# Kernel tuning notes

Measured on AMD Instinct MI355X. Metric: run time of the kernel, lower is better.

The kernel has to match this reference:

```python
import jax, jax.numpy as jnp
import numpy as np

N = 50000      # nodes
E = 800000     # edges
D_IN = 128     # input feature dim
HID = 64       # out_channels (per-head dim; concat=False -> head mean)
HEADS = 2
NEG_SLOPE = 0.2


def gat_layer(x, src, dst, Ws, Wd, a_s, a_d, b):
    # PyG GATConv, add_self_loops=False, concat=False (mean over heads)
    n = x.shape[0]
    H, C = a_s.shape
    hs = (x @ Ws).reshape(n, H, C)          # source-side features [N,H,C]
    hd = (x @ Wd).reshape(n, H, C)          # dest-side features   [N,H,C]
    als = (hs * a_s).sum(-1)                # [N,H]
    ald = (hd * a_d).sum(-1)                # [N,H]
    e = jax.nn.leaky_relu(als[src] + ald[dst], NEG_SLOPE)   # [E,H]
    # segment softmax over edges grouped by destination node
    m = jax.ops.segment_max(e, dst, num_segments=n)
    m = jax.lax.stop_gradient(jnp.where(jnp.isfinite(m), m, 0.0))
    ex = jnp.exp(e - m[dst])
    den = jax.ops.segment_sum(ex, dst, num_segments=n)
    alpha = ex / (den[dst] + 1e-16)                          # [E,H]
    out = jax.ops.segment_sum(hs[src] * alpha[:, :, None], dst, num_segments=n)
    return out.mean(axis=1) + b             # [N,C]


def setup_inputs() -> dict:
    key = jax.random.key(0)
    ks = jax.random.split(key, 32)
    d = {}
    d["x"] = jax.random.normal(ks[0], (N, D_IN), jnp.float32)
    d["edge_index"] = jax.random.randint(ks[1], (2, E), 0, N, jnp.int32)
    dins = [D_IN, HID, HID]
    i = 2
    for l in range(1, 4):
        din = dins[l - 1]
        s = 1.0 / np.sqrt(din)
        d[f"Ws{l}"] = jax.random.normal(ks[i], (din, HEADS * HID), jnp.float32) * s; i += 1
        d[f"Wd{l}"] = jax.random.normal(ks[i], (din, HEADS * HID), jnp.float32) * s; i += 1
        d[f"as{l}"] = jax.random.normal(ks[i], (HEADS, HID), jnp.float32) * 0.1; i += 1
        d[f"ad{l}"] = jax.random.normal(ks[i], (HEADS, HID), jnp.float32) * 0.1; i += 1
        d[f"b{l}"] = jnp.zeros((HID,), jnp.float32)
        d[f"Wl{l}"] = jax.random.normal(ks[i], (din, HID), jnp.float32) * s; i += 1
        d[f"bl{l}"] = jnp.zeros((HID,), jnp.float32)
    return d


def reference(x, edge_index,
              Ws1, Wd1, as1, ad1, b1, Wl1, bl1,
              Ws2, Wd2, as2, ad2, b2, Wl2, bl2,
              Ws3, Wd3, as3, ad3, b3, Wl3, bl3):
    src, dst = edge_index[0], edge_index[1]
    h = jax.nn.relu(gat_layer(x, src, dst, Ws1, Wd1, as1, ad1, b1) + x @ Wl1 + bl1)
    h = jax.nn.relu(gat_layer(h, src, dst, Ws2, Wd2, as2, ad2, b2) + h @ Wl2 + bl2)
    h = jax.nn.relu(gat_layer(h, src, dst, Ws3, Wd3, as3, ad3, b3) + h @ Wl3 + bl3)
    return h
```

## Files before the change

kernel.cpp:

```cpp
#include <hip/hip_runtime.h>
#include <hip/hip_bf16.h>

#define NN 50000
#define NE 800000
#define SCAN_BS 1024
#define SCAN_NB ((NN + SCAN_BS - 1) / SCAN_BS)
#define EB ((NE + 255) / 256)

typedef __attribute__((ext_vector_type(8))) __bf16 bf16x8;
typedef __attribute__((ext_vector_type(4))) float float4v;

__device__ __forceinline__ unsigned pack_bf2(float lo, float hi) {
    union { __bf16 b; unsigned short u; } a, c;
    a.b = (__bf16)lo; c.b = (__bf16)hi;
    return (unsigned)a.u | ((unsigned)c.u << 16);
}
__device__ __forceinline__ float2 unpack_bf2(unsigned v) {
    union { unsigned short u; __bf16 b; } lo, hi;
    lo.u = (unsigned short)(v & 0xffff); hi.u = (unsigned short)(v >> 16);
    return make_float2((float)lo.b, (float)hi.b);
}


__device__ __forceinline__ void convert_w_part(const float* __restrict__ Ws,
                                               const float* __restrict__ Wd,
                                               const float* __restrict__ Wl,
                                               __bf16* __restrict__ Wt, int K, int i)
{
    if (i >= 320 * K) return;
    int c = i / K, k = i % K;
    float v;
    if (c < 128)      v = Ws[k * 128 + c];
    else if (c < 256) v = Wd[k * 128 + (c - 128)];
    else              v = Wl[k * 64 + (c - 256)];
    Wt[i] = (__bf16)v;
}

__global__ void __launch_bounds__(256)
prep_kernel(const int* __restrict__ ei, int* __restrict__ deg, int* __restrict__ rank,
            const float* __restrict__ Ws1, const float* __restrict__ Wd1,
            const float* __restrict__ Wl1, __bf16* __restrict__ Wt1,
            const float* __restrict__ Ws2, const float* __restrict__ Wd2,
            const float* __restrict__ Wl2, __bf16* __restrict__ Wt2,
            const float* __restrict__ Ws3, const float* __restrict__ Wd3,
            const float* __restrict__ Wl3, __bf16* __restrict__ Wt3)
{
    int bi = blockIdx.x;
    if (bi < EB) {
        int e = bi * 256 + threadIdx.x;
        if (e < NE) rank[e] = atomicAdd(&deg[ei[NE + e]], 1);
    } else if (bi < EB + 160) {
        convert_w_part(Ws1, Wd1, Wl1, Wt1, 128, (bi - EB) * 256 + threadIdx.x);
    } else if (bi < EB + 240) {
        convert_w_part(Ws2, Wd2, Wl2, Wt2, 64, (bi - EB - 160) * 256 + threadIdx.x);
    } else {
        convert_w_part(Ws3, Wd3, Wl3, Wt3, 64, (bi - EB - 240) * 256 + threadIdx.x);
    }
}


__global__ void __launch_bounds__(SCAN_BS)
scan1_kernel(const int* __restrict__ deg, int* __restrict__ exl, int* __restrict__ bsum)
{
    __shared__ int sh[SCAN_BS];
    int t = threadIdx.x;
    int i = blockIdx.x * SCAN_BS + t;
    int v = (i < NN) ? deg[i] : 0;
    sh[t] = v;
    __syncthreads();
    for (int off = 1; off < SCAN_BS; off <<= 1) {
        int u = (t >= off) ? sh[t - off] : 0;
        __syncthreads();
        sh[t] += u;
        __syncthreads();
    }
    if (i < NN) exl[i] = sh[t] - v;
    if (t == SCAN_BS - 1) bsum[blockIdx.x] = sh[t];
}

__global__ void __launch_bounds__(64)
scan2_kernel(const int* __restrict__ bsum, int* __restrict__ boff, int* __restrict__ row)
{
    int l = threadIdx.x;
    int v = (l < SCAN_NB) ? bsum[l] : 0;
    int own = v;
    for (int off = 1; off < 64; off <<= 1) {
        int u = __shfl_up(v, off);
        if (l >= off) v += u;
    }
    if (l < SCAN_NB) boff[l] = v - own;
    if (l == 63) row[NN] = v;
}

__global__ void __launch_bounds__(SCAN_BS)
scan3_kernel(const int* __restrict__ exl, const int* __restrict__ boff,
             int* __restrict__ row)
{
    int i = blockIdx.x * SCAN_BS + threadIdx.x;
    if (i >= NN) return;
    row[i] = exl[i] + boff[blockIdx.x];
}

__global__ void __launch_bounds__(256)
scatter_kernel(const int* __restrict__ ei, const int* __restrict__ rank,
               const int* __restrict__ row, int* __restrict__ csr_src)
{
    int e = blockIdx.x * 256 + threadIdx.x;
    if (e >= NE) return;
    int s = ei[e], d = ei[NE + e];
    int p = row[d] + rank[e];
    csr_src[p] = s;
}


__device__ __forceinline__ bf16x8 load_af(const __bf16* p) { return *(const bf16x8*)p; }
__device__ __forceinline__ bf16x8 load_af(const float* p) {
    float4 u = *(const float4*)p;
    float4 v = *(const float4*)(p + 4);
    bf16x8 r;
    r[0] = (__bf16)u.x; r[1] = (__bf16)u.y; r[2] = (__bf16)u.z; r[3] = (__bf16)u.w;
    r[4] = (__bf16)v.x; r[5] = (__bf16)v.y; r[6] = (__bf16)v.z; r[7] = (__bf16)v.w;
    return r;
}

template <int K, typename TIN>
__global__ void __launch_bounds__(256)
mfma_gemm(const TIN* __restrict__ xin, const __bf16* __restrict__ Wt,
          const float* __restrict__ a_s, const float* __restrict__ a_d,
          unsigned* __restrict__ hsb, float* __restrict__ lin,
          float* __restrict__ als, float* __restrict__ ald)
{
    __shared__ __align__(16) char ldsW[320 * 144];

    const int tid  = threadIdx.x;
    const int lane = tid & 63;
    const int wave = tid >> 6;
    const int l15 = lane & 15, quad = lane >> 4;
    const int nblk0 = blockIdx.x * 64;
    const int n0 = nblk0 + wave * 16;
    const int nA = min(n0 + l15, NN - 1);

    bf16x8 afr[K / 32];
#pragma unroll
    for (int ks = 0; ks < K / 32; ++ks)
        afr[ks] = load_af(xin + (size_t)nA * K + ks * 32 + quad * 8);

    float4v acc[20];
#pragma unroll
    for (int t = 0; t < 20; ++t) acc[t] = (float4v){0.f, 0.f, 0.f, 0.f};

#pragma unroll
    for (int h = 0; h < K / 64; ++h) {
        uint4 tmp[10];
#pragma unroll
        for (int i = 0; i < 10; ++i) {
            int idx = i * 256 + tid;
            int r = idx >> 3, c = idx & 7;
            tmp[i] = *(const uint4*)(Wt + (size_t)r * K + h * 64 + c * 8);
        }
        if (h) __syncthreads();
#pragma unroll
        for (int i = 0; i < 10; ++i) {
            int idx = i * 256 + tid;
            int r = idx >> 3, c = idx & 7;
            *(uint4*)&ldsW[r * 144 + c * 16] = tmp[i];
        }
        __syncthreads();

#pragma unroll
        for (int ksh = 0; ksh < 2; ++ksh) {
            int ks = h * 2 + ksh;
#pragma unroll
            for (int t = 0; t < 20; ++t) {
                bf16x8 bf = *(const bf16x8*)&ldsW[(t * 16 + l15) * 144 + (ksh * 4 + quad) * 16];
                acc[t] = __builtin_amdgcn_mfma_f32_16x16x32_bf16(afr[ks], bf, acc[t], 0, 0, 0);
            }
        }
    }

    float s0[4], s1[4], d0[4], d1[4];
#pragma unroll
    for (int r = 0; r < 4; ++r) { s0[r] = 0.f; s1[r] = 0.f; d0[r] = 0.f; d1[r] = 0.f; }
#pragma unroll
    for (int t = 0; t < 4; ++t) {
        float as0 = a_s[t * 16 + l15];
        float as1 = a_s[64 + t * 16 + l15];
        float ad0 = a_d[t * 16 + l15];
        float ad1 = a_d[64 + t * 16 + l15];
#pragma unroll
        for (int r = 0; r < 4; ++r) {
            s0[r] += acc[t][r] * as0;
            s1[r] += acc[t + 4][r] * as1;
            d0[r] += acc[t + 8][r] * ad0;
            d1[r] += acc[t + 12][r] * ad1;
        }
    }
#pragma unroll
    for (int m = 1; m < 16; m <<= 1) {
#pragma unroll
        for (int r = 0; r < 4; ++r) {
            s0[r] += __shfl_xor(s0[r], m);
            s1[r] += __shfl_xor(s1[r], m);
            d0[r] += __shfl_xor(d0[r], m);
            d1[r] += __shfl_xor(d1[r], m);
        }
    }

    __syncthreads();
    unsigned* hs_l  = (unsigned*)ldsW;
    float*    lin_l = (float*)(ldsW + 64 * 68 * 4);
    float*    al_l  = (float*)(ldsW + 2 * 64 * 68 * 4);

#pragma unroll
    for (int t = 0; t < 4; ++t) {
#pragma unroll
        for (int r = 0; r < 4; ++r) {
            int ln = wave * 16 + quad * 4 + r;
            hs_l[ln * 68 + t * 16 + l15] = pack_bf2(acc[t][r], acc[t + 4][r]);
            lin_l[ln * 68 + t * 16 + l15] = acc[t + 16][r];
        }
    }
    if (l15 == 0) {
#pragma unroll
        for (int r = 0; r < 4; ++r) {
            int ln = wave * 16 + quad * 4 + r;
            al_l[0 * 64 + ln] = s0[r];
            al_l[1 * 64 + ln] = s1[r];
            al_l[2 * 64 + ln] = d0[r];
            al_l[3 * 64 + ln] = d1[r];
        }
    }
    __syncthreads();

#pragma unroll
    for (int it = 0; it < 4; ++it) {
        int idx4 = it * 256 + tid;
        int ln = idx4 >> 4, c4 = idx4 & 15;
        int n = nblk0 + ln;
        if (n < NN) {
            *(uint4*)&hsb[(size_t)n * 64 + c4 * 4] =
                *(const uint4*)&hs_l[ln * 68 + c4 * 4];
            *(float4*)&lin[(size_t)n * 64 + c4 * 4] =
                *(const float4*)&lin_l[ln * 68 + c4 * 4];
        }
    }
    {
        int half = tid >> 7;
        int t2 = tid & 127;
        int ln = t2 >> 1, h = t2 & 1;
        int n = nblk0 + ln;
        if (n < NN) {
            float v = al_l[(half * 2 + h) * 64 + ln];
            if (half == 0) als[n * 2 + h] = v;
            else           ald[n * 2 + h] = v;
        }
    }
}


__device__ __forceinline__ float2 edge_w(const float* __restrict__ als, int s,
                                         float ad0, float ad1)
{
    float2 al = *(const float2*)&als[s * 2];
    float e0 = al.x + ad0; e0 = (e0 >= 0.f) ? e0 : 0.2f * e0;
    float e1 = al.y + ad1; e1 = (e1 >= 0.f) ? e1 : 0.2f * e1;
    return make_float2(__expf(e0), __expf(e1));
}

__device__ __forceinline__ void store_q(float* p, float v0, float v1, float v2, float v3) {
    *(float4*)p = make_float4(v0, v1, v2, v3);
}
__device__ __forceinline__ void store_q(__bf16* p, float v0, float v1, float v2, float v3) {
    *(uint2*)p = make_uint2(pack_bf2(v0, v1), pack_bf2(v2, v3));
}

template <typename TO>
__global__ void __launch_bounds__(256)
gat_aggregate(const int* __restrict__ row, const int* __restrict__ csr_src,
              const float* __restrict__ als, const float* __restrict__ ald,
              const unsigned* __restrict__ hsb, const float* __restrict__ lin,
              const float* __restrict__ b, const float* __restrict__ bl,
              TO* __restrict__ out)
{
    int w = (blockIdx.x * 256 + threadIdx.x) >> 6;
    int lane = threadIdx.x & 63;
    int q = lane >> 4;
    int l15 = lane & 15;
    if (w >= NN) return;
    int p0 = row[w], p1 = row[w + 1];
    float ad0 = ald[w * 2 + 0];
    float ad1 = ald[w * 2 + 1];

    float a0[4] = {0.f, 0.f, 0.f, 0.f};
    float a1[4] = {0.f, 0.f, 0.f, 0.f};
    float den0 = 0.f, den1 = 0.f;

    int p = p0 + q;
    for (; p + 12 < p1; p += 16) {
        int sA = csr_src[p];
        int sB = csr_src[p + 4];
        int sC = csr_src[p + 8];
        int sD = csr_src[p + 12];
        float2 eA = edge_w(als, sA, ad0, ad1);
        float2 eB = edge_w(als, sB, ad0, ad1);
        float2 eC = edge_w(als, sC, ad0, ad1);
        float2 eD = edge_w(als, sD, ad0, ad1);
        uint4 gA = *(const uint4*)&hsb[(size_t)sA * 64 + 4 * l15];
        uint4 gB = *(const uint4*)&hsb[(size_t)sB * 64 + 4 * l15];
        uint4 gC = *(const uint4*)&hsb[(size_t)sC * 64 + 4 * l15];
        uint4 gD = *(const uint4*)&hsb[(size_t)sD * 64 + 4 * l15];
        den0 += (eA.x + eB.x) + (eC.x + eD.x);
        den1 += (eA.y + eB.y) + (eC.y + eD.y);
        float2 h;
        h = unpack_bf2(gA.x); a0[0] += eA.x * h.x; a1[0] += eA.y * h.y;
        h = unpack_bf2(gA.y); a0[1] += eA.x * h.x; a1[1] += eA.y * h.y;
        h = unpack_bf2(gA.z); a0[2] += eA.x * h.x; a1[2] += eA.y * h.y;
        h = unpack_bf2(gA.w); a0[3] += eA.x * h.x; a1[3] += eA.y * h.y;
        h = unpack_bf2(gB.x); a0[0] += eB.x * h.x; a1[0] += eB.y * h.y;
        h = unpack_bf2(gB.y); a0[1] += eB.x * h.x; a1[1] += eB.y * h.y;
        h = unpack_bf2(gB.z); a0[2] += eB.x * h.x; a1[2] += eB.y * h.y;
        h = unpack_bf2(gB.w); a0[3] += eB.x * h.x; a1[3] += eB.y * h.y;
        h = unpack_bf2(gC.x); a0[0] += eC.x * h.x; a1[0] += eC.y * h.y;
        h = unpack_bf2(gC.y); a0[1] += eC.x * h.x; a1[1] += eC.y * h.y;
        h = unpack_bf2(gC.z); a0[2] += eC.x * h.x; a1[2] += eC.y * h.y;
        h = unpack_bf2(gC.w); a0[3] += eC.x * h.x; a1[3] += eC.y * h.y;
        h = unpack_bf2(gD.x); a0[0] += eD.x * h.x; a1[0] += eD.y * h.y;
        h = unpack_bf2(gD.y); a0[1] += eD.x * h.x; a1[1] += eD.y * h.y;
        h = unpack_bf2(gD.z); a0[2] += eD.x * h.x; a1[2] += eD.y * h.y;
        h = unpack_bf2(gD.w); a0[3] += eD.x * h.x; a1[3] += eD.y * h.y;
    }
    for (; p + 4 < p1; p += 8) {
        int sA = csr_src[p];
        int sB = csr_src[p + 4];
        float2 eA = edge_w(als, sA, ad0, ad1);
        float2 eB = edge_w(als, sB, ad0, ad1);
        uint4 gA = *(const uint4*)&hsb[(size_t)sA * 64 + 4 * l15];
        uint4 gB = *(const uint4*)&hsb[(size_t)sB * 64 + 4 * l15];
        den0 += eA.x + eB.x;
        den1 += eA.y + eB.y;
        float2 h;
        h = unpack_bf2(gA.x); a0[0] += eA.x * h.x; a1[0] += eA.y * h.y;
        h = unpack_bf2(gA.y); a0[1] += eA.x * h.x; a1[1] += eA.y * h.y;
        h = unpack_bf2(gA.z); a0[2] += eA.x * h.x; a1[2] += eA.y * h.y;
        h = unpack_bf2(gA.w); a0[3] += eA.x * h.x; a1[3] += eA.y * h.y;
        h = unpack_bf2(gB.x); a0[0] += eB.x * h.x; a1[0] += eB.y * h.y;
        h = unpack_bf2(gB.y); a0[1] += eB.x * h.x; a1[1] += eB.y * h.y;
        h = unpack_bf2(gB.z); a0[2] += eB.x * h.x; a1[2] += eB.y * h.y;
        h = unpack_bf2(gB.w); a0[3] += eB.x * h.x; a1[3] += eB.y * h.y;
    }
    for (; p < p1; p += 4) {
        int s = csr_src[p];
        float2 e = edge_w(als, s, ad0, ad1);
        uint4 g = *(const uint4*)&hsb[(size_t)s * 64 + 4 * l15];
        den0 += e.x; den1 += e.y;
        float2 h;
        h = unpack_bf2(g.x); a0[0] += e.x * h.x; a1[0] += e.y * h.y;
        h = unpack_bf2(g.y); a0[1] += e.x * h.x; a1[1] += e.y * h.y;
        h = unpack_bf2(g.z); a0[2] += e.x * h.x; a1[2] += e.y * h.y;
        h = unpack_bf2(g.w); a0[3] += e.x * h.x; a1[3] += e.y * h.y;
    }

#pragma unroll
    for (int i = 0; i < 4; ++i) {
        a0[i] += __shfl_xor(a0[i], 16); a0[i] += __shfl_xor(a0[i], 32);
        a1[i] += __shfl_xor(a1[i], 16); a1[i] += __shfl_xor(a1[i], 32);
    }
    den0 += __shfl_xor(den0, 16); den0 += __shfl_xor(den0, 32);
    den1 += __shfl_xor(den1, 16); den1 += __shfl_xor(den1, 32);

    if (q == 0) {
        int c0 = 4 * l15;
        float r0 = 1.f / (den0 + 1e-16f);
        float r1 = 1.f / (den1 + 1e-16f);
        float4 lv = *(const float4*)&lin[(size_t)w * 64 + c0];
        float v0 = 0.5f * (a0[0] * r0 + a1[0] * r1) + b[c0 + 0] + bl[c0 + 0] + lv.x;
        float v1 = 0.5f * (a0[1] * r0 + a1[1] * r1) + b[c0 + 1] + bl[c0 + 1] + lv.y;
        float v2 = 0.5f * (a0[2] * r0 + a1[2] * r1) + b[c0 + 2] + bl[c0 + 2] + lv.z;
        float v3 = 0.5f * (a0[3] * r0 + a1[3] * r1) + b[c0 + 3] + bl[c0 + 3] + lv.w;
        store_q(&out[(size_t)w * 64 + c0],
                fmaxf(v0, 0.f), fmaxf(v1, 0.f), fmaxf(v2, 0.f), fmaxf(v3, 0.f));
    }
}


extern "C" void kernel_launch(void* const* d_in, const int* in_sizes, int n_in,
                              void* d_out, int out_size, void* d_ws, size_t ws_size,
                              hipStream_t stream)
{
    const float* x  = (const float*)d_in[0];
    const int*   ei = (const int*)d_in[1];
    const float* Ws[3]; const float* Wd[3]; const float* As[3]; const float* Ad[3];
    const float* Bb[3]; const float* Wl[3]; const float* Bl[3];
    for (int l = 0; l < 3; ++l) {
        int base = 2 + 7 * l;
        Ws[l] = (const float*)d_in[base + 0];
        Wd[l] = (const float*)d_in[base + 1];
        As[l] = (const float*)d_in[base + 2];
        Ad[l] = (const float*)d_in[base + 3];
        Bb[l] = (const float*)d_in[base + 4];
        Wl[l] = (const float*)d_in[base + 5];
        Bl[l] = (const float*)d_in[base + 6];
    }

    float* ws = (float*)d_ws;
    unsigned* hsb = (unsigned*)ws;
    float* lin  = (float*)(hsb + (size_t)NN * 64);
    float* als  = lin + (size_t)NN * 64;
    float* ald  = als + (size_t)NN * 2;
    __bf16* hb  = (__bf16*)(ald + (size_t)NN * 2);
    __bf16* Wt1 = hb + (size_t)NN * 64;
    __bf16* Wt2 = Wt1 + 320 * 128;
    __bf16* Wt3 = Wt2 + 320 * 64;
    int* row     = (int*)(Wt3 + 320 * 64);
    int* deg     = row + (NN + 1);
    int* rank    = deg + NN;
    int* exl     = rank + NE;
    int* bsum    = exl + NN;
    int* boff    = bsum + SCAN_NB;
    int* csr_src = boff + SCAN_NB;

    const int WB  = (NN * 64 + 255) / 256;
    const int GB  = (NN + 63) / 64;

    hipMemsetAsync(deg, 0, sizeof(int) * NN, stream);
    prep_kernel<<<EB + 320, 256, 0, stream>>>(ei, deg, rank,
        Ws[0], Wd[0], Wl[0], Wt1,
        Ws[1], Wd[1], Wl[1], Wt2,
        Ws[2], Wd[2], Wl[2], Wt3);
    scan1_kernel<<<SCAN_NB, SCAN_BS, 0, stream>>>(deg, exl, bsum);
    scan2_kernel<<<1, 64, 0, stream>>>(bsum, boff, row);
    scan3_kernel<<<SCAN_NB, SCAN_BS, 0, stream>>>(exl, boff, row);
    scatter_kernel<<<EB, 256, 0, stream>>>(ei, rank, row, csr_src);

    for (int l = 0; l < 3; ++l) {
        if (l == 0) {
            mfma_gemm<128, float><<<GB, 256, 0, stream>>>(
                x, Wt1, As[0], Ad[0], hsb, lin, als, ald);
        } else {
            const __bf16* wt = (l == 1) ? Wt2 : Wt3;
            mfma_gemm<64, __bf16><<<GB, 256, 0, stream>>>(
                hb, wt, As[l], Ad[l], hsb, lin, als, ald);
        }
        if (l == 2) {
            gat_aggregate<float><<<WB, 256, 0, stream>>>(
                row, csr_src, als, ald, hsb, lin, Bb[l], Bl[l], (float*)d_out);
        } else {
            gat_aggregate<__bf16><<<WB, 256, 0, stream>>>(
                row, csr_src, als, ald, hsb, lin, Bb[l], Bl[l], hb);
        }
    }
}
```

Baseline: 340.3 us.

## Fuse CSR scan stages and scatter into GEMM launch, load weights directly

Merges scan1 and scan2 into one kernel using a last-block ticket, and folds scan3 and the edge scatter into extra blocks of the first-layer GEMM launch. This removes three kernel launches and their serialization gaps. The GEMM also drops the LDS staging of weights and reads B fragments straight from global memory, relying on cache since every block reads the same small weight matrix. Risks: more global loads per MFMA and extra block types in the first GEMM grid.

```diff
diff --git a/kernel.cpp b/kernel.cpp
--- a/kernel.cpp
+++ b/kernel.cpp
@@ -6,6 +6,8 @@
 #define SCAN_BS 1024
 #define SCAN_NB ((NN + SCAN_BS - 1) / SCAN_BS)
 #define EB ((NE + 255) / 256)
+#define GB ((NN + 63) / 64)
+#define RB ((NN + 1 + 255) / 256)
 
 typedef __attribute__((ext_vector_type(8))) __bf16 bf16x8;
 typedef __attribute__((ext_vector_type(4))) float float4v;
@@ -60,9 +62,11 @@
 
 
 __global__ void __launch_bounds__(SCAN_BS)
-scan1_kernel(const int* __restrict__ deg, int* __restrict__ exl, int* __restrict__ bsum)
+scan12_kernel(const int* __restrict__ deg, int* __restrict__ exl,
+              int* __restrict__ bsum, int* __restrict__ boff, int* __restrict__ ticket)
 {
     __shared__ int sh[SCAN_BS];
+    __shared__ int lastFlag;
     int t = threadIdx.x;
     int i = blockIdx.x * SCAN_BS + t;
     int v = (i < NN) ? deg[i] : 0;
@@ -75,41 +79,23 @@
         __syncthreads();
     }
     if (i < NN) exl[i] = sh[t] - v;
-    if (t == SCAN_BS - 1) bsum[blockIdx.x] = sh[t];
-}
-
-__global__ void __launch_bounds__(64)
-scan2_kernel(const int* __restrict__ bsum, int* __restrict__ boff, int* __restrict__ row)
-{
-    int l = threadIdx.x;
-    int v = (l < SCAN_NB) ? bsum[l] : 0;
-    int own = v;
-    for (int off = 1; off < 64; off <<= 1) {
-        int u = __shfl_up(v, off);
-        if (l >= off) v += u;
-    }
-    if (l < SCAN_NB) boff[l] = v - own;
-    if (l == 63) row[NN] = v;
-}
-
-__global__ void __launch_bounds__(SCAN_BS)
-scan3_kernel(const int* __restrict__ exl, const int* __restrict__ boff,
-             int* __restrict__ row)
-{
-    int i = blockIdx.x * SCAN_BS + threadIdx.x;
-    if (i >= NN) return;
-    row[i] = exl[i] + boff[blockIdx.x];
-}
-
-__global__ void __launch_bounds__(256)
-scatter_kernel(const int* __restrict__ ei, const int* __restrict__ rank,
-               const int* __restrict__ row, int* __restrict__ csr_src)
-{
-    int e = blockIdx.x * 256 + threadIdx.x;
-    if (e >= NE) return;
-    int s = ei[e], d = ei[NE + e];
-    int p = row[d] + rank[e];
-    csr_src[p] = s;
+    if (t == SCAN_BS - 1) {
+        bsum[blockIdx.x] = sh[t];
+        __threadfence();
+        lastFlag = (atomicAdd(ticket, 1) == SCAN_NB - 1);
+    }
+    __syncthreads();
+    if (lastFlag && t < 64) {
+        __threadfence();
+        int l = t;
+        int bv = (l < SCAN_NB) ? bsum[l] : 0;
+        int own = bv;
+        for (int off = 1; off < 64; off <<= 1) {
+            int u = __shfl_up(bv, off);
+            if (l >= off) bv += u;
+        }
+        if (l < SCAN_NB) boff[l] = bv - own;
+    }
 }
 
 
@@ -123,16 +109,36 @@
     return r;
 }
 
-template <int K, typename TIN>
+template <int K, typename TIN, bool FUSE>
 __global__ void __launch_bounds__(256)
 mfma_gemm(const TIN* __restrict__ xin, const __bf16* __restrict__ Wt,
           const float* __restrict__ a_s, const float* __restrict__ a_d,
           unsigned* __restrict__ hsb, float* __restrict__ lin,
-          float* __restrict__ als, float* __restrict__ ald)
-{
-    __shared__ __align__(16) char ldsW[320 * 144];
-
-    const int tid  = threadIdx.x;
+          float* __restrict__ als, float* __restrict__ ald,
+          const int* __restrict__ ei, const int* __restrict__ rank,
+          const int* __restrict__ exl, const int* __restrict__ boff,
+          int* __restrict__ row, int* __restrict__ csr_src)
+{
+    const int tid = threadIdx.x;
+
+    if (FUSE && blockIdx.x >= GB) {
+        int bi = blockIdx.x - GB;
+        if (bi < RB) {
+            int i = bi * 256 + tid;
+            if (i < NN)       row[i] = exl[i] + boff[i >> 10];
+            else if (i == NN) row[i] = NE;
+        } else {
+            int e = (bi - RB) * 256 + tid;
+            if (e < NE) {
+                int s = ei[e], d = ei[NE + e];
+                csr_src[exl[d] + boff[d >> 10] + rank[e]] = s;
+            }
+        }
+        return;
+    }
+
+    __shared__ __align__(16) char ldsE[2 * 64 * 68 * 4 + 1024];
+
     const int lane = tid & 63;
     const int wave = tid >> 6;
     const int l15 = lane & 15, quad = lane >> 4;
@@ -149,32 +155,13 @@
 #pragma unroll
     for (int t = 0; t < 20; ++t) acc[t] = (float4v){0.f, 0.f, 0.f, 0.f};
 
-#pragma unroll
-    for (int h = 0; h < K / 64; ++h) {
-        uint4 tmp[10];
-#pragma unroll
-        for (int i = 0; i < 10; ++i) {
-            int idx = i * 256 + tid;
-            int r = idx >> 3, c = idx & 7;
-            tmp[i] = *(const uint4*)(Wt + (size_t)r * K + h * 64 + c * 8);
-        }
-        if (h) __syncthreads();
-#pragma unroll
-        for (int i = 0; i < 10; ++i) {
-            int idx = i * 256 + tid;
-            int r = idx >> 3, c = idx & 7;
-            *(uint4*)&ldsW[r * 144 + c * 16] = tmp[i];
-        }
-        __syncthreads();
-
-#pragma unroll
-        for (int ksh = 0; ksh < 2; ++ksh) {
-            int ks = h * 2 + ksh;
-#pragma unroll
-            for (int t = 0; t < 20; ++t) {
-                bf16x8 bf = *(const bf16x8*)&ldsW[(t * 16 + l15) * 144 + (ksh * 4 + quad) * 16];
-                acc[t] = __builtin_amdgcn_mfma_f32_16x16x32_bf16(afr[ks], bf, acc[t], 0, 0, 0);
-            }
+    const __bf16* bp = Wt + (size_t)l15 * K + quad * 8;
+#pragma unroll
+    for (int ks = 0; ks < K / 32; ++ks) {
+#pragma unroll
+        for (int t = 0; t < 20; ++t) {
+            bf16x8 bf = *(const bf16x8*)(bp + (size_t)t * 16 * K + ks * 32);
+            acc[t] = __builtin_amdgcn_mfma_f32_16x16x32_bf16(afr[ks], bf, acc[t], 0, 0, 0);
         }
     }
 
@@ -206,10 +193,9 @@
         }
     }
 
-    __syncthreads();
-    unsigned* hs_l  = (unsigned*)ldsW;
-    float*    lin_l = (float*)(ldsW + 64 * 68 * 4);
-    float*    al_l  = (float*)(ldsW + 2 * 64 * 68 * 4);
+    unsigned* hs_l  = (unsigned*)ldsE;
+    float*    lin_l = (float*)(ldsE + 64 * 68 * 4);
+    float*    al_l  = (float*)(ldsE + 2 * 64 * 68 * 4);
 
 #pragma unroll
     for (int t = 0; t < 4; ++t) {
@@ -413,33 +399,32 @@
     __bf16* Wt3 = Wt2 + 320 * 64;
     int* row     = (int*)(Wt3 + 320 * 64);
     int* deg     = row + (NN + 1);
-    int* rank    = deg + NN;
+    int* ticket  = deg + NN;
+    int* rank    = ticket + 1;
     int* exl     = rank + NE;
     int* bsum    = exl + NN;
     int* boff    = bsum + SCAN_NB;
     int* csr_src = boff + SCAN_NB;
 
-    const int WB  = (NN * 64 + 255) / 256;
-    const int GB  = (NN + 63) / 64;
-
-    hipMemsetAsync(deg, 0, sizeof(int) * NN, stream);
+    const int WB = (NN * 64 + 255) / 256;
+
+    hipMemsetAsync(deg, 0, sizeof(int) * (NN + 1), stream);
     prep_kernel<<<EB + 320, 256, 0, stream>>>(ei, deg, rank,
         Ws[0], Wd[0], Wl[0], Wt1,
         Ws[1], Wd[1], Wl[1], Wt2,
         Ws[2], Wd[2], Wl[2], Wt3);
-    scan1_kernel<<<SCAN_NB, SCAN_BS, 0, stream>>>(deg, exl, bsum);
-    scan2_kernel<<<1, 64, 0, stream>>>(bsum, boff, row);
-    scan3_kernel<<<SCAN_NB, SCAN_BS, 0, stream>>>(exl, boff, row);
-    scatter_kernel<<<EB, 256, 0, stream>>>(ei, rank, row, csr_src);
+    scan12_kernel<<<SCAN_NB, SCAN_BS, 0, stream>>>(deg, exl, bsum, boff, ticket);
 
     for (int l = 0; l < 3; ++l) {
         if (l == 0) {
-            mfma_gemm<128, float><<<GB, 256, 0, stream>>>(
-                x, Wt1, As[0], Ad[0], hsb, lin, als, ald);
+            mfma_gemm<128, float, true><<<GB + RB + EB, 256, 0, stream>>>(
+                x, Wt1, As[0], Ad[0], hsb, lin, als, ald,
+                ei, rank, exl, boff, row, csr_src);
         } else {
             const __bf16* wt = (l == 1) ? Wt2 : Wt3;
-            mfma_gemm<64, __bf16><<<GB, 256, 0, stream>>>(
-                hb, wt, As[l], Ad[l], hsb, lin, als, ald);
+            mfma_gemm<64, __bf16, false><<<GB, 256, 0, stream>>>(
+                hb, wt, As[l], Ad[l], hsb, lin, als, ald,
+                nullptr, nullptr, nullptr, nullptr, nullptr, nullptr);
         }
         if (l == 2) {
             gat_aggregate<float><<<WB, 256, 0, stream>>>(
```

Result: slower. 367.1 us (+7.9%).
